# Performance work log

Measured on AMD Instinct MI355X. Metric: run time of the kernel, lower is better.

The kernel has to match this reference:

```python
import jax, jax.numpy as jnp
import numpy as np

D_MODEL = 768
NUM_HEADS = 12
HEAD_DIM = D_MODEL // NUM_HEADS
ROPE_THETA = 10000.0
MAX_SEQ_LEN = 2048
BATCH = 2
SEQ = 2048


def _rope_tables():
    # powers = arange(0, d_k, 2)/d_k ; freqs = theta**-powers ; angles = t outer freqs
    powers = jnp.arange(0, HEAD_DIM, 2, dtype=jnp.float32) / HEAD_DIM
    freqs = 1.0 / (ROPE_THETA ** powers)                      # [d_k/2]
    t = jnp.arange(MAX_SEQ_LEN, dtype=jnp.float32)
    angles = t[:, None] * freqs[None, :]                      # [max_seq_len, d_k/2]
    return jnp.cos(angles), jnp.sin(angles)


def _apply_rope(x, cos, sin, pos):
    # x: [b, h, s, d], pos: [b, s]; interleaved even/odd pairing
    c = cos[pos][:, None]          # [b, 1, s, d/2]
    s = sin[pos][:, None]
    x_even = x[..., 0::2]
    x_odd = x[..., 1::2]
    new_even = x_even * c - x_odd * s
    new_odd = x_even * s + x_odd * c
    # re-interleave: (..., f, 2) -> (..., 2f)
    return jnp.stack([new_even, new_odd], axis=-1).reshape(x.shape)


def setup_inputs() -> dict:
    key = jax.random.key(0)
    k1, k2, k3 = jax.random.split(key, 3)
    x = jax.random.normal(k1, (BATCH, SEQ, D_MODEL), dtype=jnp.float32)
    token_positions = jnp.broadcast_to(jnp.arange(SEQ, dtype=jnp.int32), (BATCH, SEQ))
    sigma_qkv = (2.0 / (D_MODEL + 3 * D_MODEL)) ** 0.5
    sigma_o = (2.0 / (D_MODEL + D_MODEL)) ** 0.5
    W_qkv = jax.random.normal(k2, (3 * D_MODEL, D_MODEL), dtype=jnp.float32) * sigma_qkv
    W_o = jax.random.normal(k3, (D_MODEL, D_MODEL), dtype=jnp.float32) * sigma_o
    return {"x": x, "token_positions": token_positions, "W_qkv": W_qkv, "W_o": W_o}


def reference(x, token_positions, W_qkv, W_o):
    b, s, _ = x.shape
    cos, sin = _rope_tables()
    qkv = jnp.einsum('bsd,ed->bse', x, W_qkv)                 # [b, s, 3*d_model]
    qkv = qkv.reshape(b, s, 3, NUM_HEADS, HEAD_DIM)
    qkv = jnp.transpose(qkv, (2, 0, 3, 1, 4))                 # [3, b, h, s, hd]
    q, k, v = qkv[0], qkv[1], qkv[2]
    q = _apply_rope(q, cos, sin, token_positions)
    k = _apply_rope(k, cos, sin, token_positions)
    scores = jnp.einsum('bhqd,bhkd->bhqk', q, k) / (HEAD_DIM ** 0.5)
    causal = jnp.tril(jnp.ones((s, s), dtype=bool))
    scores = jnp.where(causal, scores, -jnp.inf)
    weights = jax.nn.softmax(scores, axis=-1)
    context = jnp.einsum('bhqk,bhkd->bhqd', weights, v)
    context = jnp.transpose(context, (0, 2, 1, 3)).reshape(b, s, D_MODEL)
    return jnp.einsum('bsd,ed->bse', context, W_o)
```

## Files before the change

kernel.cpp:

```cpp
#include <hip/hip_runtime.h>
#include <hip/hip_bf16.h>
#include <math.h>

#define SEQ 2048
#define DM 768
#define NH 12
#define HD 64
#define NB 2
#define NT (NB*SEQ)
#define E3 (3*DM)

using short4v = __attribute__((ext_vector_type(4))) short;
using short8v = __attribute__((ext_vector_type(8))) short;
using floatx4 = __attribute__((ext_vector_type(4))) float;
using int4v   = __attribute__((ext_vector_type(4))) int;

#if __has_builtin(__builtin_amdgcn_exp2f)
#define EXPFN(x) __builtin_amdgcn_exp2f(x)
#define QSCALE 0.1803368801111244f
#else
#define EXPFN(x) __expf(x)
#define QSCALE 0.125f
#endif

static __device__ __forceinline__ short bfb(float f) {
  union { __hip_bfloat16 h; short s; } u;
  u.h = __float2bfloat16(f);
  return u.s;
}

static __device__ __forceinline__ void gload_lds16(const __hip_bfloat16* g, __hip_bfloat16* lds) {
  __builtin_amdgcn_global_load_lds(
      (const __attribute__((address_space(1))) unsigned int*)g,
      (__attribute__((address_space(3))) unsigned int*)lds, 16, 0, 0);
}

static __device__ __forceinline__ int swzg(int row) {
  return (((row >> 3) & 3) + 2 * (row & 3)) & 7;
}

#define XN4 (NT * DM / 4)
#define WQN4 (E3 * DM / 4)
#define WON4 (DM * DM / 4)
#define CVT_N (XN4 + WQN4 + WON4)
__global__ void cvt3_rope(const float* __restrict__ x, const float* __restrict__ wq,
                          const float* __restrict__ wo,
                          __hip_bfloat16* __restrict__ xb, __hip_bfloat16* __restrict__ wqb,
                          __hip_bfloat16* __restrict__ wob, float2* __restrict__ rcs,
                          int* __restrict__ qcnt) {
  int i = blockIdx.x * blockDim.x + threadIdx.x;
  if (blockIdx.x == 0 && threadIdx.x < 8) qcnt[threadIdx.x] = 0;
  if (i >= CVT_N) {
    int idx = i - CVT_N;
    if (idx < SEQ * 32) {
      int pos = idx >> 5, j = idx & 31;
      float freq = __expf(-(float)j * (logf(10000.0f) / 32.0f));
      float ang = (float)pos * freq;
      rcs[idx] = make_float2(cosf(ang), sinf(ang));
    }
    return;
  }
  const float* src;
  __hip_bfloat16* dst;
  int k;
  if (i < XN4) { src = x; dst = xb; k = i; }
  else if (i < XN4 + WQN4) { src = wq; dst = wqb; k = i - XN4; }
  else { src = wo; dst = wob; k = i - XN4 - WQN4; }
  floatx4 v = ((const floatx4*)src)[k];
  short4v o;
  o[0] = bfb(v[0]); o[1] = bfb(v[1]); o[2] = bfb(v[2]); o[3] = bfb(v[3]);
  ((short4v*)dst)[k] = o;
}

__global__ __launch_bounds__(256) void qkv_gemm_rope(
    const __hip_bfloat16* __restrict__ Wq,
    const __hip_bfloat16* __restrict__ Xb,
    const int* __restrict__ tpos,
    const float2* __restrict__ rcs,
    __hip_bfloat16* __restrict__ Qb, __hip_bfloat16* __restrict__ Kb,
    __hip_bfloat16* __restrict__ Vt)
{
  __shared__ __align__(16) __hip_bfloat16 As[64 * 128];
  __shared__ __align__(16) __hip_bfloat16 Bs[128 * 128];
  const int tid = threadIdx.x;
  const int lane = tid & 63, w = tid >> 6;
  const int c = lane & 15, g = lane >> 4;
  const int wr = w >> 1, wc = w & 1;
  const int bid = blockIdx.x;
  const int xcd = bid & 7, i_ = bid >> 3;
  const int nb = xcd * 4 + (i_ & 3), mb = i_ >> 2;
  const int m0 = mb * 64, n0 = nb * 128;
  const int srow = tid >> 4, sslot = tid & 15;

  floatx4 acc[2][4] = {};
  for (int k0 = 0; k0 < DM; k0 += 128) {
#pragma unroll
    for (int j = 0; j < 4; ++j) {
      const int row = j * 16 + srow;
      const int gs = (sslot ^ (row & 15)) * 8;
      gload_lds16(Wq + (size_t)(m0 + row) * DM + k0 + gs, As + j * 2048 + w * 512);
    }
#pragma unroll
    for (int j = 0; j < 8; ++j) {
      const int row = j * 16 + srow;
      const int gs = (sslot ^ (row & 15)) * 8;
      gload_lds16(Xb + (size_t)(n0 + row) * DM + k0 + gs, Bs + j * 2048 + w * 512);
    }
    __syncthreads();
#pragma unroll
    for (int kk = 0; kk < 4; ++kk) {
      short8v a[2], b[4];
#pragma unroll
      for (int i = 0; i < 2; ++i) {
        const int row = wr * 32 + i * 16 + c;
        a[i] = *(const short8v*)&As[row * 128 + (((kk * 4 + g) ^ (row & 15)) * 8)];
      }
#pragma unroll
      for (int j = 0; j < 4; ++j) {
        const int row = wc * 64 + j * 16 + c;
        b[j] = *(const short8v*)&Bs[row * 128 + (((kk * 4 + g) ^ (row & 15)) * 8)];
      }
#pragma unroll
      for (int i = 0; i < 2; ++i)
#pragma unroll
        for (int j = 0; j < 4; ++j)
          acc[i][j] = __builtin_amdgcn_mfma_f32_16x16x32_bf16(a[i], b[j], acc[i][j], 0, 0, 0);
    }
    __syncthreads();
  }
#pragma unroll
  for (int i = 0; i < 2; ++i) {
    const int e0 = m0 + wr * 32 + i * 16 + 4 * g;
    const int jj = (e0 & 63) >> 1;
#pragma unroll
    for (int j = 0; j < 4; ++j) {
      const int t = n0 + wc * 64 + j * 16 + c;
      const int b_ = t >> 11, s = t & (SEQ - 1);
      float v0 = acc[i][j][0], v1 = acc[i][j][1], v2 = acc[i][j][2], v3 = acc[i][j][3];
      if (e0 < 2 * DM) {
        const int pos = tpos[t];
        const float2 cs0 = rcs[pos * 32 + jj];
        const float2 cs1 = rcs[pos * 32 + jj + 1];
        const float n0v = v0 * cs0.x - v1 * cs0.y, n1v = v0 * cs0.y + v1 * cs0.x;
        const float n2v = v2 * cs1.x - v3 * cs1.y, n3v = v2 * cs1.y + v3 * cs1.x;
        v0 = n0v; v1 = n1v; v2 = n2v; v3 = n3v;
      }
      if (e0 < DM) {
        const int h = e0 >> 6, d = e0 & 63;
        short4v pk;
        pk[0] = bfb(v0 * QSCALE); pk[1] = bfb(v1 * QSCALE);
        pk[2] = bfb(v2 * QSCALE); pk[3] = bfb(v3 * QSCALE);
        *(short4v*)&Qb[(((size_t)(b_ * NH + h) * SEQ) + s) * HD + d] = pk;
      } else if (e0 < 2 * DM) {
        const int e = e0 - DM, h = e >> 6, d = e & 63;
        short4v pk;
        pk[0] = bfb(v0); pk[1] = bfb(v1); pk[2] = bfb(v2); pk[3] = bfb(v3);
        *(short4v*)&Kb[(((size_t)(b_ * NH + h) * SEQ) + s) * HD + d] = pk;
      } else {
        const int e = e0 - 2 * DM, h = e >> 6, d = e & 63;
        const size_t base = ((size_t)(b_ * NH + h) * HD + d) * SEQ + s;
        Vt[base]           = __float2bfloat16(v0);
        Vt[base + SEQ]     = __float2bfloat16(v1);
        Vt[base + 2 * SEQ] = __float2bfloat16(v2);
        Vt[base + 3 * SEQ] = __float2bfloat16(v3);
      }
    }
  }
}

__global__ __launch_bounds__(512) void attn_fused(
    const __hip_bfloat16* __restrict__ Qb,
    const __hip_bfloat16* __restrict__ Kb,
    const __hip_bfloat16* __restrict__ Vt,
    __hip_bfloat16* __restrict__ Cx,
    int* __restrict__ qcnt)
{
  __shared__ __align__(16) __hip_bfloat16 Ks[2][128 * 64];
  __shared__ __align__(16) __hip_bfloat16 Vs[2][64 * 128];
  __shared__ int task_s;
  const int tid = threadIdx.x;
  const int lane = tid & 63, w = tid >> 6;
  const int c = lane & 15, g = lane >> 4;
  const int xcd = blockIdx.x & 7;
  const int kr1 = 8 * (c >> 2) + (c & 3);
  const int ksr = w * 8 + (lane >> 3), kss = lane & 7;
  const int vsr = w * 4 + (lane >> 4), vss = lane & 15;

  for (;;) {
    if (tid == 0) task_s = atomicAdd(&qcnt[xcd], 1);
    __syncthreads();
    const int task = task_s;
    if (task >= 48) return;
    const int qG = 15 - task / 3;
    const int bh = xcd + 8 * (task % 3);
    const int KBmax = qG;
    const __hip_bfloat16* Qh = Qb + (size_t)bh * SEQ * HD;
    const __hip_bfloat16* Kh = Kb + (size_t)bh * SEQ * HD;
    const __hip_bfloat16* Vh = Vt + (size_t)bh * HD * SEQ;
    const int q1 = qG * 128 + w * 16 + c;
    const int qt_w = 4 * qG + (w >> 1);
    const int qrl32 = (w & 1) * 16 + c;
    const short8v qf10 = *(const short8v*)&Qh[(size_t)q1 * HD + g * 8];
    const short8v qf11 = *(const short8v*)&Qh[(size_t)q1 * HD + 32 + g * 8];
    floatx4 o1[4] = {};
    float l1 = 0.0f;

#define STAGE_KV(KB_, KSD, VSD)                                                      \
    do {                                                                             \
      _Pragma("unroll")                                                              \
      for (int j = 0; j < 2; ++j) {                                                  \
        const int kr = j * 64 + ksr;                                                 \
        gload_lds16(Kh + (size_t)((KB_) * 128 + kr) * HD + ((kss ^ swzg(kr)) * 8),   \
                    (KSD) + j * 4096 + w * 512);                                     \
        const int vr = j * 32 + vsr;                                                 \
        gload_lds16(Vh + (size_t)vr * SEQ + (KB_) * 128 + ((vss ^ (vr & 15)) * 8),   \
                    (VSD) + j * 4096 + w * 512);                                     \
      }                                                                              \
    } while (0)

    STAGE_KV(0, Ks[0], Vs[0]);
    __syncthreads();
    int cb = 0;
    for (int kb = 0; kb <= KBmax; ++kb) {
      if (kb < KBmax) STAGE_KV(kb + 1, Ks[cb ^ 1], Vs[cb ^ 1]);
      {
        const __hip_bfloat16* Kt = Ks[cb];
        const __hip_bfloat16* Vb = Vs[cb];
#pragma unroll
        for (int s = 0; s < 4; ++s) {
          const int kidx = 4 * kb + s;
          if (kidx <= qt_w) {
            const int r0 = s * 32 + kr1, r1 = r0 + 4;
            const int z0 = swzg(r0), z1 = swzg(r1);
            const short8v a00 = *(const short8v*)&Kt[r0 * 64 + ((g ^ z0) * 8)];
            const short8v a01 = *(const short8v*)&Kt[r0 * 64 + (((4 + g) ^ z0) * 8)];
            const short8v a10 = *(const short8v*)&Kt[r1 * 64 + ((g ^ z1) * 8)];
            const short8v a11 = *(const short8v*)&Kt[r1 * 64 + (((4 + g) ^ z1) * 8)];
            short8v vf[4];
#pragma unroll
            for (int f = 0; f < 4; ++f) {
              const int rv = f * 16 + c;
              vf[f] = *(const short8v*)&Vb[rv * 128 + (((s * 4 + g) ^ (rv & 15)) * 8)];
            }
            floatx4 s1a = {}, s1b = {};
            s1a = __builtin_amdgcn_mfma_f32_16x16x32_bf16(a00, qf10, s1a, 0, 0, 0);
            s1a = __builtin_amdgcn_mfma_f32_16x16x32_bf16(a01, qf11, s1a, 0, 0, 0);
            s1b = __builtin_amdgcn_mfma_f32_16x16x32_bf16(a10, qf10, s1b, 0, 0, 0);
            s1b = __builtin_amdgcn_mfma_f32_16x16x32_bf16(a11, qf11, s1b, 0, 0, 0);
            if (kidx == qt_w) {
#pragma unroll
              for (int r = 0; r < 4; ++r) {
                if (8 * g + r > qrl32) s1a[r] = -INFINITY;
                if (8 * g + r + 4 > qrl32) s1b[r] = -INFINITY;
              }
            }
            short8v pf1;
#pragma unroll
            for (int r = 0; r < 4; ++r) {
              float p;
              p = EXPFN(s1a[r]); l1 += p; pf1[r] = bfb(p);
              p = EXPFN(s1b[r]); l1 += p; pf1[r + 4] = bfb(p);
            }
            o1[0] = __builtin_amdgcn_mfma_f32_16x16x32_bf16(vf[0], pf1, o1[0], 0, 0, 0);
            o1[1] = __builtin_amdgcn_mfma_f32_16x16x32_bf16(vf[1], pf1, o1[1], 0, 0, 0);
            o1[2] = __builtin_amdgcn_mfma_f32_16x16x32_bf16(vf[2], pf1, o1[2], 0, 0, 0);
            o1[3] = __builtin_amdgcn_mfma_f32_16x16x32_bf16(vf[3], pf1, o1[3], 0, 0, 0);
          }
        }
      }
      __syncthreads();
      cb ^= 1;
    }
#undef STAGE_KV

    l1 += __shfl_xor(l1, 16); l1 += __shfl_xor(l1, 32);
    const float inv1 = 1.0f / l1;
    const int bb = bh / NH, h = bh - bb * NH;
    const size_t trow1 = ((size_t)bb * SEQ + q1) * DM + (size_t)h * HD;
#pragma unroll
    for (int f = 0; f < 4; ++f) {
      short4v pk1;
#pragma unroll
      for (int r = 0; r < 4; ++r) pk1[r] = bfb(o1[f][r] * inv1);
      *(short4v*)&Cx[trow1 + f * 16 + 4 * g] = pk1;
    }
  }
}

__global__ __launch_bounds__(256) void out_gemm(
    const __hip_bfloat16* __restrict__ Wo,
    const __hip_bfloat16* __restrict__ Cx,
    float* __restrict__ out)
{
  __shared__ __align__(16) __hip_bfloat16 As[64 * 128];
  __shared__ __align__(16) __hip_bfloat16 Bs[128 * 128];
  const int tid = threadIdx.x;
  const int lane = tid & 63, w = tid >> 6;
  const int c = lane & 15, g = lane >> 4;
  const int wr = w >> 1, wc = w & 1;
  const int bid = blockIdx.x;
  const int xcd = bid & 7, i_ = bid >> 3;
  const int nb = xcd * 4 + (i_ & 3), mb = i_ >> 2;
  const int m0 = mb * 64, n0 = nb * 128;
  const int srow = tid >> 4, sslot = tid & 15;

  floatx4 acc[2][4] = {};
  for (int k0 = 0; k0 < DM; k0 += 128) {
#pragma unroll
    for (int j = 0; j < 4; ++j) {
      const int row = j * 16 + srow;
      const int gs = (sslot ^ (row & 15)) * 8;
      gload_lds16(Wo + (size_t)(m0 + row) * DM + k0 + gs, As + j * 2048 + w * 512);
    }
#pragma unroll
    for (int j = 0; j < 8; ++j) {
      const int row = j * 16 + srow;
      const int gs = (sslot ^ (row & 15)) * 8;
      gload_lds16(Cx + (size_t)(n0 + row) * DM + k0 + gs, Bs + j * 2048 + w * 512);
    }
    __syncthreads();
#pragma unroll
    for (int kk = 0; kk < 4; ++kk) {
      short8v a[2], b[4];
#pragma unroll
      for (int i = 0; i < 2; ++i) {
        const int row = wr * 32 + i * 16 + c;
        a[i] = *(const short8v*)&As[row * 128 + (((kk * 4 + g) ^ (row & 15)) * 8)];
      }
#pragma unroll
      for (int j = 0; j < 4; ++j) {
        const int row = wc * 64 + j * 16 + c;
        b[j] = *(const short8v*)&Bs[row * 128 + (((kk * 4 + g) ^ (row & 15)) * 8)];
      }
#pragma unroll
      for (int i = 0; i < 2; ++i)
#pragma unroll
        for (int j = 0; j < 4; ++j)
          acc[i][j] = __builtin_amdgcn_mfma_f32_16x16x32_bf16(a[i], b[j], acc[i][j], 0, 0, 0);
    }
    __syncthreads();
  }
#pragma unroll
  for (int i = 0; i < 2; ++i) {
    const int e0 = m0 + wr * 32 + i * 16 + 4 * g;
#pragma unroll
    for (int j = 0; j < 4; ++j) {
      const int t = n0 + wc * 64 + j * 16 + c;
      *(floatx4*)&out[(size_t)t * DM + e0] = acc[i][j];
    }
  }
}

extern "C" void kernel_launch(void* const* d_in, const int* in_sizes, int n_in,
                              void* d_out, int out_size, void* d_ws, size_t ws_size,
                              hipStream_t stream) {
  const float* x    = (const float*)d_in[0];
  const int*   tpos = (const int*)d_in[1];
  const float* Wq   = (const float*)d_in[2];
  const float* Wo   = (const float*)d_in[3];
  float* out = (float*)d_out;

  const size_t QKV_BYTES = (size_t)NB * NH * SEQ * HD * 2;
  const size_t REQUIRED = 4 * QKV_BYTES;
  if (ws_size < REQUIRED) return;

  char* ws = (char*)d_ws;
  __hip_bfloat16* Qb = (__hip_bfloat16*)(ws);
  __hip_bfloat16* Kb = (__hip_bfloat16*)(ws + QKV_BYTES);
  __hip_bfloat16* Vt = (__hip_bfloat16*)(ws + 2 * QKV_BYTES);
  __hip_bfloat16* Cx = (__hip_bfloat16*)(ws + 3 * QKV_BYTES);
  __hip_bfloat16* xb = (__hip_bfloat16*)(ws + 3 * QKV_BYTES);
  char* ob = (char*)d_out;
  float2* rcs = (float2*)(ob);
  __hip_bfloat16* wqb = (__hip_bfloat16*)(ob + (size_t)SEQ * 32 * 8);
  __hip_bfloat16* wob = (__hip_bfloat16*)(ob + (size_t)SEQ * 32 * 8 + (size_t)E3 * DM * 2);
  int* qcnt = (int*)(ob + (size_t)SEQ * 32 * 8 + (size_t)E3 * DM * 2 + (size_t)DM * DM * 2);

  const int TOT_N = CVT_N + SEQ * 32;
  cvt3_rope<<<dim3((TOT_N + 255) / 256), dim3(256), 0, stream>>>(x, Wq, Wo, xb, wqb, wob, rcs, qcnt);
  qkv_gemm_rope<<<dim3(1152), dim3(256), 0, stream>>>(wqb, xb, tpos, rcs, Qb, Kb, Vt);
  attn_fused<<<dim3(512), dim3(512), 0, stream>>>(Qb, Kb, Vt, Cx, qcnt);
  out_gemm<<<dim3(384), dim3(256), 0, stream>>>(wob, Cx, out);
}
```

Measured before the change: 87.19 us.

## Double-buffer LDS tiles in QKV and output GEMMs with BK=64

Both projection GEMMs now use two LDS buffers with a K-step of 64 instead of one buffer with K-step 128. The next K tile is prefetched asynchronously while the current one feeds the MFMAs, so global-load latency can overlap compute. Shared memory footprint stays the same, but there are twice as many K iterations and barriers per block. The attention kernel, which probably dominates runtime, is unchanged.

```diff
diff --git a/kernel.cpp b/kernel.cpp
--- a/kernel.cpp
+++ b/kernel.cpp
@@ -80,8 +80,8 @@
     __hip_bfloat16* __restrict__ Qb, __hip_bfloat16* __restrict__ Kb,
     __hip_bfloat16* __restrict__ Vt)
 {
-  __shared__ __align__(16) __hip_bfloat16 As[64 * 128];
-  __shared__ __align__(16) __hip_bfloat16 Bs[128 * 128];
+  __shared__ __align__(16) __hip_bfloat16 As[2][64 * 64];
+  __shared__ __align__(16) __hip_bfloat16 Bs[2][128 * 64];
   const int tid = threadIdx.x;
   const int lane = tid & 63, w = tid >> 6;
   const int c = lane & 15, g = lane >> 4;
@@ -90,35 +90,42 @@
   const int xcd = bid & 7, i_ = bid >> 3;
   const int nb = xcd * 4 + (i_ & 3), mb = i_ >> 2;
   const int m0 = mb * 64, n0 = nb * 128;
-  const int srow = tid >> 4, sslot = tid & 15;
+  const int srow = tid >> 3, sslot = tid & 7;
+
+#define QKV_STAGE(K0_, AD, BD)                                                      \
+  do {                                                                              \
+    _Pragma("unroll")                                                               \
+    for (int j = 0; j < 2; ++j) {                                                   \
+      const int row = j * 32 + srow;                                                \
+      const int gs = (sslot ^ (row & 7)) * 8;                                       \
+      gload_lds16(Wq + (size_t)(m0 + row) * DM + (K0_) + gs, (AD) + j * 2048 + w * 512); \
+    }                                                                               \
+    _Pragma("unroll")                                                               \
+    for (int j = 0; j < 4; ++j) {                                                   \
+      const int row = j * 32 + srow;                                                \
+      const int gs = (sslot ^ (row & 7)) * 8;                                       \
+      gload_lds16(Xb + (size_t)(n0 + row) * DM + (K0_) + gs, (BD) + j * 2048 + w * 512); \
+    }                                                                               \
+  } while (0)
 
   floatx4 acc[2][4] = {};
-  for (int k0 = 0; k0 < DM; k0 += 128) {
-#pragma unroll
-    for (int j = 0; j < 4; ++j) {
-      const int row = j * 16 + srow;
-      const int gs = (sslot ^ (row & 15)) * 8;
-      gload_lds16(Wq + (size_t)(m0 + row) * DM + k0 + gs, As + j * 2048 + w * 512);
-    }
-#pragma unroll
-    for (int j = 0; j < 8; ++j) {
-      const int row = j * 16 + srow;
-      const int gs = (sslot ^ (row & 15)) * 8;
-      gload_lds16(Xb + (size_t)(n0 + row) * DM + k0 + gs, Bs + j * 2048 + w * 512);
-    }
-    __syncthreads();
-#pragma unroll
-    for (int kk = 0; kk < 4; ++kk) {
+  QKV_STAGE(0, As[0], Bs[0]);
+  int cb = 0;
+  for (int k0 = 0; k0 < DM; k0 += 64) {
+    if (k0 + 64 < DM) QKV_STAGE(k0 + 64, As[cb ^ 1], Bs[cb ^ 1]);
+    __syncthreads();
+#pragma unroll
+    for (int kk = 0; kk < 2; ++kk) {
       short8v a[2], b[4];
 #pragma unroll
       for (int i = 0; i < 2; ++i) {
         const int row = wr * 32 + i * 16 + c;
-        a[i] = *(const short8v*)&As[row * 128 + (((kk * 4 + g) ^ (row & 15)) * 8)];
+        a[i] = *(const short8v*)&As[cb][row * 64 + (((kk * 4 + g) ^ (row & 7)) * 8)];
       }
 #pragma unroll
       for (int j = 0; j < 4; ++j) {
         const int row = wc * 64 + j * 16 + c;
-        b[j] = *(const short8v*)&Bs[row * 128 + (((kk * 4 + g) ^ (row & 15)) * 8)];
+        b[j] = *(const short8v*)&Bs[cb][row * 64 + (((kk * 4 + g) ^ (row & 7)) * 8)];
       }
 #pragma unroll
       for (int i = 0; i < 2; ++i)
@@ -127,7 +134,9 @@
           acc[i][j] = __builtin_amdgcn_mfma_f32_16x16x32_bf16(a[i], b[j], acc[i][j], 0, 0, 0);
     }
     __syncthreads();
-  }
+    cb ^= 1;
+  }
+#undef QKV_STAGE
 #pragma unroll
   for (int i = 0; i < 2; ++i) {
     const int e0 = m0 + wr * 32 + i * 16 + 4 * g;
@@ -292,8 +301,8 @@
     const __hip_bfloat16* __restrict__ Cx,
     float* __restrict__ out)
 {
-  __shared__ __align__(16) __hip_bfloat16 As[64 * 128];
-  __shared__ __align__(16) __hip_bfloat16 Bs[128 * 128];
+  __shared__ __align__(16) __hip_bfloat16 As[2][64 * 64];
+  __shared__ __align__(16) __hip_bfloat16 Bs[2][128 * 64];
   const int tid = threadIdx.x;
   const int lane = tid & 63, w = tid >> 6;
   const int c = lane & 15, g = lane >> 4;
@@ -302,35 +311,42 @@
   const int xcd = bid & 7, i_ = bid >> 3;
   const int nb = xcd * 4 + (i_ & 3), mb = i_ >> 2;
   const int m0 = mb * 64, n0 = nb * 128;
-  const int srow = tid >> 4, sslot = tid & 15;
+  const int srow = tid >> 3, sslot = tid & 7;
+
+#define OUT_STAGE(K0_, AD, BD)                                                      \
+  do {                                                                              \
+    _Pragma("unroll")                                                               \
+    for (int j = 0; j < 2; ++j) {                                                   \
+      const int row = j * 32 + srow;                                                \
+      const int gs = (sslot ^ (row & 7)) * 8;                                       \
+      gload_lds16(Wo + (size_t)(m0 + row) * DM + (K0_) + gs, (AD) + j * 2048 + w * 512); \
+    }                                                                               \
+    _Pragma("unroll")                                                               \
+    for (int j = 0; j < 4; ++j) {                                                   \
+      const int row = j * 32 + srow;                                                \
+      const int gs = (sslot ^ (row & 7)) * 8;                                       \
+      gload_lds16(Cx + (size_t)(n0 + row) * DM + (K0_) + gs, (BD) + j * 2048 + w * 512); \
+    }                                                                               \
+  } while (0)
 
   floatx4 acc[2][4] = {};
-  for (int k0 = 0; k0 < DM; k0 += 128) {
-#pragma unroll
-    for (int j = 0; j < 4; ++j) {
-      const int row = j * 16 + srow;
-      const int gs = (sslot ^ (row & 15)) * 8;
-      gload_lds16(Wo + (size_t)(m0 + row) * DM + k0 + gs, As + j * 2048 + w * 512);
-    }
-#pragma unroll
-    for (int j = 0; j < 8; ++j) {
-      const int row = j * 16 + srow;
-      const int gs = (sslot ^ (row & 15)) * 8;
-      gload_lds16(Cx + (size_t)(n0 + row) * DM + k0 + gs, Bs + j * 2048 + w * 512);
-    }
-    __syncthreads();
-#pragma unroll
-    for (int kk = 0; kk < 4; ++kk) {
+  OUT_STAGE(0, As[0], Bs[0]);
+  int cb = 0;
+  for (int k0 = 0; k0 < DM; k0 += 64) {
+    if (k0 + 64 < DM) OUT_STAGE(k0 + 64, As[cb ^ 1], Bs[cb ^ 1]);
+    __syncthreads();
+#pragma unroll
+    for (int kk = 0; kk < 2; ++kk) {
       short8v a[2], b[4];
 #pragma unroll
       for (int i = 0; i < 2; ++i) {
         const int row = wr * 32 + i * 16 + c;
-        a[i] = *(const short8v*)&As[row * 128 + (((kk * 4 + g) ^ (row & 15)) * 8)];
+        a[i] = *(const short8v*)&As[cb][row * 64 + (((kk * 4 + g) ^ (row & 7)) * 8)];
       }
 #pragma unroll
       for (int j = 0; j < 4; ++j) {
         const int row = wc * 64 + j * 16 + c;
-        b[j] = *(const short8v*)&Bs[row * 128 + (((kk * 4 + g) ^ (row & 15)) * 8)];
+        b[j] = *(const short8v*)&Bs[cb][row * 64 + (((kk * 4 + g) ^ (row & 7)) * 8)];
       }
 #pragma unroll
       for (int i = 0; i < 2; ++i)
@@ -339,7 +355,9 @@
           acc[i][j] = __builtin_amdgcn_mfma_f32_16x16x32_bf16(a[i], b[j], acc[i][j], 0, 0, 0);
     }
     __syncthreads();
-  }
+    cb ^= 1;
+  }
+#undef OUT_STAGE
 #pragma unroll
   for (int i = 0; i < 2; ++i) {
     const int e0 = m0 + wr * 32 + i * 16 + 4 * g;
```

After: 87.03 us. No clear change (-0.2%).
